# Performance work log

Measured on AMD Instinct MI355X. Metric: run time of the kernel, lower is better.

The kernel has to match this reference:

```python
import jax, jax.numpy as jnp
import numpy as np

B, T = 128, 512
V, E, U, K = 50000, 100, 128, 32


def _lstm(x, Wk, Wr, b):
    # x: [B, T, D] -> [B, T, U], Keras LSTM gate order i,f,g,o
    Bd = x.shape[0]
    Ud = Wr.shape[0]
    xs = jnp.swapaxes(x, 0, 1)  # [T, B, D]

    def step(carry, xt):
        h, c = carry
        z = xt @ Wk + h @ Wr + b
        i, f, g, o = jnp.split(z, 4, axis=-1)
        c = jax.nn.sigmoid(f) * c + jax.nn.sigmoid(i) * jnp.tanh(g)
        h = jax.nn.sigmoid(o) * jnp.tanh(c)
        return (h, c), h

    init = (jnp.zeros((Bd, Ud), x.dtype), jnp.zeros((Bd, Ud), x.dtype))
    _, hs = jax.lax.scan(step, init, xs)
    return jnp.swapaxes(hs, 0, 1)


def _crf_logZ(em, trans):
    # em: [B, T, K] emissions; trans: [K, K]. Forward algorithm log-partition.
    alpha0 = em[:, 0]  # [B, K]
    es = jnp.swapaxes(em[:, 1:], 0, 1)  # [T-1, B, K]

    def step(alpha, et):
        # alpha[b, i] + trans[i, j] -> logsumexp over i, plus emission
        alpha = jax.nn.logsumexp(alpha[:, :, None] + trans[None], axis=1) + et
        return alpha, None

    alphaT, _ = jax.lax.scan(step, alpha0, es)
    return jax.nn.logsumexp(alphaT, axis=-1)  # [B]


def setup_inputs() -> dict:
    key = jax.random.key(0)
    ks = jax.random.split(key, 11)
    s = 0.1
    return {
        "tokens": jax.random.randint(ks[0], (B, T), 0, V, dtype=jnp.int32),
        "emb": jax.random.normal(ks[1], (V, E), jnp.float32) * s,
        "Wk_f": jax.random.normal(ks[2], (E, 4 * U), jnp.float32) * s,
        "Wr_f": jax.random.normal(ks[3], (U, 4 * U), jnp.float32) * s,
        "b_f": jnp.zeros((4 * U,), jnp.float32),
        "Wk_b": jax.random.normal(ks[4], (E, 4 * U), jnp.float32) * s,
        "Wr_b": jax.random.normal(ks[5], (U, 4 * U), jnp.float32) * s,
        "b_b": jnp.zeros((4 * U,), jnp.float32),
        "crf_kernel": jax.random.normal(ks[6], (2 * U, K), jnp.float32) * s,
        "crf_bias": jnp.zeros((K,), jnp.float32),
        "trans": jax.random.normal(ks[7], (K, K), jnp.float32) * s,
    }


def reference(tokens, emb, Wk_f, Wr_f, b_f, Wk_b, Wr_b, b_b, crf_kernel, crf_bias, trans):
    x = emb[tokens]  # [B, T, E]
    h_f = _lstm(x, Wk_f, Wr_f, b_f)
    h_b = _lstm(x[:, ::-1], Wk_b, Wr_b, b_b)[:, ::-1]
    h = jnp.concatenate([h_f, h_b], axis=-1)  # [B, T, 2U] (dropout = identity at inference)
    em = h @ crf_kernel + crf_bias  # [B, T, K] CRF emission potentials
    return _crf_logZ(em, trans)  # [B] log-partition via CRF forward DP
```

## Files before the change

### kernel.cpp

```cpp
#include <hip/hip_runtime.h>
#include <hip/hip_bf16.h>

#define B_  128
#define T_  512
#define V_  50000
#define VP  50016
#define E_  100
#define U_  128
#define K_  32
#define G4  512
#define KP  128
#define GRP 8

typedef _Float16 h2_t __attribute__((ext_vector_type(2)));
typedef _Float16 f16x8 __attribute__((ext_vector_type(8)));
typedef __fp16   h2raw_t __attribute__((ext_vector_type(2)));
typedef short    bf16x8 __attribute__((ext_vector_type(8)));
typedef float    f32x4  __attribute__((ext_vector_type(4)));
typedef unsigned short u16x4 __attribute__((ext_vector_type(4)));

__device__ __forceinline__ h2_t pk2(float a, float b) {
    h2raw_t r = __builtin_amdgcn_cvt_pkrtz(a, b);
    union { h2raw_t r; h2_t h; } u; u.r = r; return u.h;
}

#if __has_builtin(__builtin_amdgcn_rcpf)
__device__ __forceinline__ float rcp_f(float x) { return __builtin_amdgcn_rcpf(x); }
#else
__device__ __forceinline__ float rcp_f(float x) { return 1.f / x; }
#endif

__device__ __forceinline__ unsigned short bf16_bits(float v) {
    __hip_bfloat16 b = __float2bfloat16(v);
    union { __hip_bfloat16 b; unsigned short s; } u; u.b = b; return u.s;
}
__device__ __forceinline__ float bf2f(unsigned short u) {
    union { unsigned int i; float f; } x; x.i = ((unsigned int)u) << 16; return x.f;
}

__global__ __launch_bounds__(128) void pack_b_kernel(
    const float* __restrict__ Wk_f, const float* __restrict__ Wk_b,
    __hip_bfloat16* __restrict__ Bb)
{
    const int n = blockIdx.x;
    const int k = threadIdx.x;
    float v = 0.f;
    if (k < E_) v = (n < 512) ? Wk_f[k * 512 + n] : Wk_b[k * 512 + (n - 512)];
    Bb[n * KP + k] = __float2bfloat16(v);
}

__global__ __launch_bounds__(256, 2) void proj_mfma_kernel(
    const float* __restrict__ emb,
    const __hip_bfloat16* __restrict__ Bb,
    const float* __restrict__ b_f, const float* __restrict__ b_b,
    __hip_bfloat16* __restrict__ proj)
{
    const int r0   = blockIdx.x * 32;
    const int tid  = threadIdx.x;
    const int wv   = tid >> 6;
    const int lane = tid & 63;
    const int quad = lane >> 4;
    const int l16  = lane & 15;

    __shared__ __align__(16) float C_lds[32][268];
    unsigned short* A_st = (unsigned short*)&C_lds[0][0];

    for (int idx = tid; idx < 32 * 64; idx += 256) {
        int r = idx >> 6, kk = idx & 63;
        int vr = r0 + r; if (vr >= V_) vr = V_ - 1;
        unsigned int w = 0;
        if (kk < 50) {
            float2 v = *(const float2*)(emb + (long long)vr * E_ + 2 * kk);
            w = ((unsigned int)bf16_bits(v.y) << 16) | bf16_bits(v.x);
        }
        *(unsigned int*)&A_st[r * 136 + 2 * kk] = w;
    }
    __syncthreads();

    bf16x8 af[2][4];
    #pragma unroll
    for (int mt = 0; mt < 2; ++mt)
        #pragma unroll
        for (int kc = 0; kc < 4; ++kc)
            af[mt][kc] = *(const bf16x8*)&A_st[(mt * 16 + l16) * 136 +
                                               kc * 32 + quad * 8];
    __syncthreads();

    const unsigned short* Bu = (const unsigned short*)Bb;

    for (int ng = 0; ng < 4; ++ng) {
        const int n0 = ng * 256;

        bf16x8 bfr[4][4];
        #pragma unroll
        for (int nt = 0; nt < 4; ++nt)
            #pragma unroll
            for (int kc = 0; kc < 4; ++kc)
                bfr[nt][kc] = *(const bf16x8*)(Bu +
                    (n0 + wv * 64 + nt * 16 + l16) * KP + kc * 32 + quad * 8);

        f32x4 acc[2][4];
        #pragma unroll
        for (int mt = 0; mt < 2; ++mt)
            #pragma unroll
            for (int nt = 0; nt < 4; ++nt)
                acc[mt][nt] = (f32x4){0.f, 0.f, 0.f, 0.f};

        #pragma unroll
        for (int mt = 0; mt < 2; ++mt)
            #pragma unroll
            for (int nt = 0; nt < 4; ++nt)
                #pragma unroll
                for (int kc = 0; kc < 4; ++kc)
                    acc[mt][nt] = __builtin_amdgcn_mfma_f32_16x16x32_bf16(
                        af[mt][kc], bfr[nt][kc], acc[mt][nt], 0, 0, 0);

        #pragma unroll
        for (int mt = 0; mt < 2; ++mt)
            #pragma unroll
            for (int nt = 0; nt < 4; ++nt)
                #pragma unroll
                for (int v = 0; v < 4; ++v)
                    C_lds[mt * 16 + quad * 4 + v][wv * 64 + nt * 16 + l16] =
                        acc[mt][nt][v];
        __syncthreads();

        const float* bias = (n0 < 512) ? b_f : b_b;
        const int nbase = n0 & 511;
        for (int idx = tid; idx < 32 * 128; idx += 256) {
            int r = idx >> 7, cc = (idx & 127) * 2;
            float v0 = C_lds[r][cc]     + bias[nbase + cc];
            float v1 = C_lds[r][cc + 1] + bias[nbase + cc + 1];
            unsigned int w = ((unsigned int)bf16_bits(v1) << 16) | bf16_bits(v0);
            *(unsigned int*)(proj + (long long)(r0 + r) * 1024 + n0 + cc) = w;
        }
        __syncthreads();
    }
}

__device__ __forceinline__ float sigmoid_f(float x) {
    return rcp_f(1.f + __expf(-x));
}
__device__ __forceinline__ float tanh_f(float x) {
    return 1.f - 2.f * rcp_f(__expf(2.f * x) + 1.f);
}

__global__ __launch_bounds__(512, 1) void lstm_kernel(
    const __hip_bfloat16* __restrict__ proj,
    const int* __restrict__ tokens,
    const float* __restrict__ Wr_f, const float* __restrict__ Wr_b,
    __hip_bfloat16* __restrict__ h_buf)
{
    const int bid  = blockIdx.x;
    const int dir  = bid >> 7;
    const int b    = bid & 127;
    const int tid  = threadIdx.x;
    const int w    = tid >> 6;
    const int lane = tid & 63;
    const int quad = lane >> 4;
    const int l16  = lane & 15;
    const int unit = 16 * w + l16;

    const float* Wr = dir ? Wr_b : Wr_f;

    union uf16 { f16x8 v; h2_t p[4]; };
    f16x8 wb[4][4];
    #pragma unroll
    for (int gq = 0; gq < 4; ++gq) {
        const int col = gq * 128 + unit;
        #pragma unroll
        for (int kc = 0; kc < 4; ++kc) {
            const int k0 = kc * 32 + quad * 8;
            uf16 u;
            #pragma unroll
            for (int jj = 0; jj < 4; ++jj)
                u.p[jj] = pk2(Wr[(k0 + 2 * jj)     * G4 + col],
                              Wr[(k0 + 2 * jj + 1) * G4 + col]);
            wb[gq][kc] = u.v;
        }
    }

    __shared__ __align__(16) _Float16 hpl[2][128];
    __shared__ __align__(16) unsigned short xkl[2][GRP][512];
    if (tid < 128) hpl[0][tid] = (_Float16)0.f;
    float c = 0.f;

    const int tbase = b * T_;
    const long long rowbase = (long long)b * T_;
    const __hip_bfloat16* prt = proj + dir * 512 + tid;
    const int xw = (tid & 127) * 4 + (tid >> 7);

    int tokn[GRP];
    {
        unsigned short v0[GRP];
        #pragma unroll
        for (int d = 0; d < GRP; ++d) {
            int t0 = dir ? (T_ - 1 - d) : d;
            int tk = tokens[tbase + t0];
            v0[d] = *(const unsigned short*)(prt + (long long)tk * 1024);
        }
        #pragma unroll
        for (int d = 0; d < GRP; ++d)
            xkl[0][d][xw] = v0[d];
        #pragma unroll
        for (int d = 0; d < GRP; ++d) {
            int s = GRP + d;
            int t1 = dir ? (T_ - 1 - s) : s;
            tokn[d] = tokens[tbase + t1];
        }
    }
    __syncthreads();

    const int NG = T_ / GRP;
    for (int g = 0; g < NG; ++g) {
        unsigned short xknx[GRP];
        #pragma unroll
        for (int d = 0; d < GRP; ++d)
            xknx[d] = *(const unsigned short*)(prt + (long long)tokn[d] * 1024);

        int tokn2[GRP];
        #pragma unroll
        for (int d = 0; d < GRP; ++d) {
            int s = (g + 2) * GRP + d; if (s > T_ - 1) s = T_ - 1;
            int t = dir ? (T_ - 1 - s) : s;
            tokn2[d] = tokens[tbase + t];
        }

        float hreg[GRP];
        #pragma unroll
        for (int d = 0; d < GRP; ++d) {
            f16x8 a[4];
            #pragma unroll
            for (int kc = 0; kc < 4; ++kc)
                a[kc] = *(const f16x8*)&hpl[d & 1][kc * 32 + quad * 8];

            u16x4 xr = *(const u16x4*)&xkl[g & 1][d][(unsigned)unit * 4];

            f32x4 acc[4];
            #pragma unroll
            for (int gq = 0; gq < 4; ++gq)
                acc[gq] = (f32x4){0.f, 0.f, 0.f, 0.f};
            #pragma unroll
            for (int gq = 0; gq < 4; ++gq)
                #pragma unroll
                for (int kc = 0; kc < 4; ++kc)
                    acc[gq] = __builtin_amdgcn_mfma_f32_16x16x32_f16(
                        a[kc], wb[gq][kc], acc[gq], 0, 0, 0);

            float zi = acc[0][0] + bf2f(xr.x);
            float zf = acc[1][0] + bf2f(xr.y);
            float zg = acc[2][0] + bf2f(xr.z);
            float zo = acc[3][0] + bf2f(xr.w);
            c = sigmoid_f(zf) * c + sigmoid_f(zi) * tanh_f(zg);
            float h = sigmoid_f(zo) * tanh_f(c);
            hreg[d] = h;

            if (quad == 0) hpl[(d + 1) & 1][unit] = (_Float16)h;

            if (d < GRP - 1) {
                asm volatile("s_waitcnt lgkmcnt(0)" ::: "memory");
                __builtin_amdgcn_s_barrier();
                asm volatile("" ::: "memory");
            } else {
                #pragma unroll
                for (int dd = 0; dd < GRP; ++dd)
                    xkl[(g + 1) & 1][dd][xw] = xknx[dd];
                asm volatile("s_waitcnt lgkmcnt(0)" ::: "memory");
                __builtin_amdgcn_s_barrier();
                asm volatile("" ::: "memory");
            }
        }

        unsigned int hp[GRP];
        #pragma unroll
        for (int d = 0; d < GRP; ++d) {
            float hn = __shfl_down(hreg[d], 1, 64);
            hp[d] = ((unsigned int)bf16_bits(hn) << 16) | bf16_bits(hreg[d]);
        }
        if (quad == 0 && !(l16 & 1)) {
            #pragma unroll
            for (int d = 0; d < GRP; ++d) {
                int s = g * GRP + d;
                int t = dir ? (T_ - 1 - s) : s;
                *(unsigned int*)(h_buf + (rowbase + t) * 256 + dir * U_ + unit) =
                    hp[d];
            }
        }

        #pragma unroll
        for (int d = 0; d < GRP; ++d) tokn[d] = tokn2[d];
    }
}

__global__ __launch_bounds__(256) void em_kernel(
    const __hip_bfloat16* __restrict__ h_buf,
    const float* __restrict__ ck, const float* __restrict__ cb,
    float* __restrict__ em)
{
    const int tid  = threadIdx.x;
    const int part = tid >> 5;
    const int k    = tid & 31;

    float ckr[32];
    #pragma unroll
    for (int i = 0; i < 32; ++i)
        ckr[i] = ck[(part * 32 + i) * K_ + k];
    const float cbk = cb[k];

    __shared__ float h_l[8][256];
    __shared__ float part_l[8][8][K_];

    const int r0 = blockIdx.x * 64;

    for (int round = 0; round < 8; ++round) {
        const int rbase = r0 + round * 8;
        #pragma unroll
        for (int j = 0; j < 8; ++j)
            h_l[j][tid] = __bfloat162float(h_buf[(long long)(rbase + j) * 256 + tid]);
        __syncthreads();

        #pragma unroll
        for (int j = 0; j < 8; ++j) {
            float pp = 0.f;
            #pragma unroll
            for (int i = 0; i < 32; ++i)
                pp = fmaf(h_l[j][part * 32 + i], ckr[i], pp);
            part_l[j][part][k] = pp;
        }
        __syncthreads();

        {
            int j2 = tid >> 5;
            float e = cbk;
            #pragma unroll
            for (int pq = 0; pq < 8; ++pq) e += part_l[j2][pq][k];
            em[(long long)(rbase + j2) * K_ + k] = e;
        }
        __syncthreads();
    }
}

#define PF_ 8
__global__ __launch_bounds__(64) void crf_kernel(
    const float* __restrict__ em,
    const float* __restrict__ trans,
    float* __restrict__ out)
{
    const int b    = blockIdx.x;
    const int lane = threadIdx.x;
    const int k    = lane & 31;
    const int half = lane >> 5;

    float etr[16];
    #pragma unroll
    for (int i = 0; i < 16; ++i)
        etr[i] = __expf(trans[(half * 16 + i) * K_ + k]);

    const float* em_b = em + (long long)b * T_ * K_;

    float ep[PF_];
    #pragma unroll
    for (int d = 0; d < PF_; ++d)
        ep[d] = em_b[d * K_ + k];

    float w = 0.f;
    float L = 0.f;
    for (int tb = 0; tb < T_; tb += PF_) {
        float en[PF_];
        if (tb + PF_ < T_) {
            #pragma unroll
            for (int d = 0; d < PF_; ++d)
                en[d] = em_b[(tb + PF_ + d) * K_ + k];
        } else {
            #pragma unroll
            for (int d = 0; d < PF_; ++d) en[d] = 0.f;
        }

        float eem[PF_];
        #pragma unroll
        for (int d = 0; d < PF_; ++d) eem[d] = __expf(ep[d]);

        #pragma unroll
        for (int d = 0; d < PF_; ++d) {
            if (tb + d == 0) {
                w = eem[d];
            } else {
                float acc = 0.f;
                #pragma unroll
                for (int i = 0; i < 16; ++i) {
                    float wv = __shfl(w, half * 16 + i, 64);
                    acc = fmaf(wv, etr[i], acc);
                }
                acc += __shfl_xor(acc, 32, 64);
                w = acc * eem[d];
            }
        }

        {
            float w0 = __shfl(w, 0, 64);
            w *= rcp_f(w0);
            L += __logf(w0);
        }

        #pragma unroll
        for (int d = 0; d < PF_; ++d) ep[d] = en[d];
    }

    float s = w;
    #pragma unroll
    for (int d = 1; d < 32; d <<= 1)
        s += __shfl_xor(s, d, 64);
    if (lane == 0) out[b] = L + __logf(s);
}

extern "C" void kernel_launch(void* const* d_in, const int* in_sizes, int n_in,
                              void* d_out, int out_size, void* d_ws, size_t ws_size,
                              hipStream_t stream)
{
    const int*   tokens = (const int*)  d_in[0];
    const float* emb    = (const float*)d_in[1];
    const float* Wk_f   = (const float*)d_in[2];
    const float* Wr_f   = (const float*)d_in[3];
    const float* b_f    = (const float*)d_in[4];
    const float* Wk_b   = (const float*)d_in[5];
    const float* Wr_b   = (const float*)d_in[6];
    const float* b_b    = (const float*)d_in[7];
    const float* ck     = (const float*)d_in[8];
    const float* cb     = (const float*)d_in[9];
    const float* trans  = (const float*)d_in[10];
    float* out = (float*)d_out;

    const long long ROWS = (long long)B_ * T_;
    __hip_bfloat16* proj  = (__hip_bfloat16*)d_ws;
    __hip_bfloat16* h_buf = proj + (long long)VP * 1024;
    float* em = (float*)(h_buf + ROWS * 256);
    __hip_bfloat16* Bb = (__hip_bfloat16*)(em + ROWS * K_);

    hipLaunchKernelGGL(pack_b_kernel, dim3(1024), dim3(128), 0, stream,
                       Wk_f, Wk_b, Bb);
    hipLaunchKernelGGL(proj_mfma_kernel, dim3(VP / 32), dim3(256), 0, stream,
                       emb, Bb, b_f, b_b, proj);
    hipLaunchKernelGGL(lstm_kernel, dim3(256), dim3(512), 0, stream,
                       proj, tokens, Wr_f, Wr_b, h_buf);
    hipLaunchKernelGGL(em_kernel, dim3((int)(ROWS / 64)), dim3(256), 0, stream,
                       h_buf, ck, cb, em);
    hipLaunchKernelGGL(crf_kernel, dim3(B_), dim3(64), 0, stream,
                       em, trans, out);
}
```

Baseline: 575.7 us.

## Batch 16 sequences per LSTM block to fill MFMA rows

The LSTM kernel now processes 16 batch rows per workgroup instead of one, so all 16 rows of each 16x16x32 MFMA carry real hidden states rather than one useful row. The grid shrinks from 256 to 16 blocks, cutting redundant recurrent matmul work per sequence. Input-projection gathers are restaged per timestep into a transposed LDS layout, with one barrier per step. The cost is that only 16 CUs are used, so the whole 512-step serial chain runs on far fewer compute units.

```diff
diff --git a/kernel.cpp b/kernel.cpp
--- a/kernel.cpp
+++ b/kernel.cpp
@@ -10,7 +10,6 @@
 #define K_  32
 #define G4  512
 #define KP  128
-#define GRP 8
 
 typedef _Float16 h2_t __attribute__((ext_vector_type(2)));
 typedef _Float16 f16x8 __attribute__((ext_vector_type(8)));
@@ -152,8 +151,8 @@
     __hip_bfloat16* __restrict__ h_buf)
 {
     const int bid  = blockIdx.x;
-    const int dir  = bid >> 7;
-    const int b    = bid & 127;
+    const int dir  = bid >> 3;
+    const int b0   = (bid & 7) * 16;
     const int tid  = threadIdx.x;
     const int w    = tid >> 6;
     const int lane = tid & 63;
@@ -180,115 +179,115 @@
         }
     }
 
-    __shared__ __align__(16) _Float16 hpl[2][128];
-    __shared__ __align__(16) unsigned short xkl[2][GRP][512];
-    if (tid < 128) hpl[0][tid] = (_Float16)0.f;
-    float c = 0.f;
-
-    const int tbase = b * T_;
-    const long long rowbase = (long long)b * T_;
-    const __hip_bfloat16* prt = proj + dir * 512 + tid;
-    const int xw = (tid & 127) * 4 + (tid >> 7);
-
-    int tokn[GRP];
+    __shared__ __align__(16) _Float16      h_lds[2][16][136];
+    __shared__ __align__(16) unsigned short xkb[2][128][72];
+
+    const int cp   = tid >> 1;
+    const int cgrp = (tid & 1) * 8;
+    const int col0 = cp * 2;
+    const int g0   = col0 >> 7;
+    const int u0   = col0 & 127;
+    const unsigned short* prj = (const unsigned short*)proj + dir * 512 + col0;
+
+    for (int idx = tid; idx < 16 * 136; idx += 512)
+        ((_Float16*)h_lds[0])[idx] = (_Float16)0.f;
+    float cst[4] = {0.f, 0.f, 0.f, 0.f};
+
+    int tokS[8];
     {
-        unsigned short v0[GRP];
-        #pragma unroll
-        for (int d = 0; d < GRP; ++d) {
-            int t0 = dir ? (T_ - 1 - d) : d;
-            int tk = tokens[tbase + t0];
-            v0[d] = *(const unsigned short*)(prt + (long long)tk * 1024);
-        }
-        #pragma unroll
-        for (int d = 0; d < GRP; ++d)
-            xkl[0][d][xw] = v0[d];
-        #pragma unroll
-        for (int d = 0; d < GRP; ++d) {
-            int s = GRP + d;
-            int t1 = dir ? (T_ - 1 - s) : s;
-            tokn[d] = tokens[tbase + t1];
-        }
+        const int tt0 = dir ? (T_ - 1) : 0;
+        int v32[8];
+        #pragma unroll
+        for (int cc = 0; cc < 8; ++cc) {
+            int tk = tokens[(b0 + cgrp + cc) * T_ + tt0];
+            v32[cc] = *(const int*)(prj + (size_t)tk * 1024);
+        }
+        union { unsigned short s[8]; uint4 q; } plo, phi;
+        #pragma unroll
+        for (int cc = 0; cc < 8; ++cc) {
+            plo.s[cc] = (unsigned short)(v32[cc] & 0xffff);
+            phi.s[cc] = (unsigned short)(((unsigned int)v32[cc]) >> 16);
+        }
+        *(uint4*)&xkb[0][u0][g0 * 16 + cgrp]     = plo.q;
+        *(uint4*)&xkb[0][u0 + 1][g0 * 16 + cgrp] = phi.q;
+        const int tt1 = dir ? (T_ - 2) : 1;
+        #pragma unroll
+        for (int cc = 0; cc < 8; ++cc)
+            tokS[cc] = tokens[(b0 + cgrp + cc) * T_ + tt1];
     }
     __syncthreads();
 
-    const int NG = T_ / GRP;
-    for (int g = 0; g < NG; ++g) {
-        unsigned short xknx[GRP];
-        #pragma unroll
-        for (int d = 0; d < GRP; ++d)
-            xknx[d] = *(const unsigned short*)(prt + (long long)tokn[d] * 1024);
-
-        int tokn2[GRP];
-        #pragma unroll
-        for (int d = 0; d < GRP; ++d) {
-            int s = (g + 2) * GRP + d; if (s > T_ - 1) s = T_ - 1;
-            int t = dir ? (T_ - 1 - s) : s;
-            tokn2[d] = tokens[tbase + t];
-        }
-
-        float hreg[GRP];
-        #pragma unroll
-        for (int d = 0; d < GRP; ++d) {
-            f16x8 a[4];
+    for (int t = 0; t < T_; ++t) {
+        const int cb = t & 1, nb = cb ^ 1;
+
+        int v32[8];
+        #pragma unroll
+        for (int cc = 0; cc < 8; ++cc)
+            v32[cc] = *(const int*)(prj + (size_t)tokS[cc] * 1024);
+
+        int tokN[8];
+        {
+            int s2 = (t + 2 < T_) ? (t + 2) : (T_ - 1);
+            int tt2 = dir ? (T_ - 1 - s2) : s2;
+            #pragma unroll
+            for (int cc = 0; cc < 8; ++cc)
+                tokN[cc] = tokens[(b0 + cgrp + cc) * T_ + tt2];
+        }
+
+        f16x8 a[4];
+        #pragma unroll
+        for (int kc = 0; kc < 4; ++kc)
+            a[kc] = *(const f16x8*)&h_lds[cb][l16][kc * 32 + quad * 8];
+        u16x4 xr[4];
+        #pragma unroll
+        for (int gq = 0; gq < 4; ++gq)
+            xr[gq] = *(const u16x4*)&xkb[cb][unit][gq * 16 + quad * 4];
+
+        f32x4 acc[4];
+        #pragma unroll
+        for (int gq = 0; gq < 4; ++gq)
+            acc[gq] = (f32x4){0.f, 0.f, 0.f, 0.f};
+        #pragma unroll
+        for (int gq = 0; gq < 4; ++gq)
             #pragma unroll
             for (int kc = 0; kc < 4; ++kc)
-                a[kc] = *(const f16x8*)&hpl[d & 1][kc * 32 + quad * 8];
-
-            u16x4 xr = *(const u16x4*)&xkl[g & 1][d][(unsigned)unit * 4];
-
-            f32x4 acc[4];
-            #pragma unroll
-            for (int gq = 0; gq < 4; ++gq)
-                acc[gq] = (f32x4){0.f, 0.f, 0.f, 0.f};
-            #pragma unroll
-            for (int gq = 0; gq < 4; ++gq)
-                #pragma unroll
-                for (int kc = 0; kc < 4; ++kc)
-                    acc[gq] = __builtin_amdgcn_mfma_f32_16x16x32_f16(
-                        a[kc], wb[gq][kc], acc[gq], 0, 0, 0);
-
-            float zi = acc[0][0] + bf2f(xr.x);
-            float zf = acc[1][0] + bf2f(xr.y);
-            float zg = acc[2][0] + bf2f(xr.z);
-            float zo = acc[3][0] + bf2f(xr.w);
-            c = sigmoid_f(zf) * c + sigmoid_f(zi) * tanh_f(zg);
-            float h = sigmoid_f(zo) * tanh_f(c);
-            hreg[d] = h;
-
-            if (quad == 0) hpl[(d + 1) & 1][unit] = (_Float16)h;
-
-            if (d < GRP - 1) {
-                asm volatile("s_waitcnt lgkmcnt(0)" ::: "memory");
-                __builtin_amdgcn_s_barrier();
-                asm volatile("" ::: "memory");
-            } else {
-                #pragma unroll
-                for (int dd = 0; dd < GRP; ++dd)
-                    xkl[(g + 1) & 1][dd][xw] = xknx[dd];
-                asm volatile("s_waitcnt lgkmcnt(0)" ::: "memory");
-                __builtin_amdgcn_s_barrier();
-                asm volatile("" ::: "memory");
+                acc[gq] = __builtin_amdgcn_mfma_f32_16x16x32_f16(
+                    a[kc], wb[gq][kc], acc[gq], 0, 0, 0);
+
+        float hb[4];
+        #pragma unroll
+        for (int v = 0; v < 4; ++v) {
+            float zi = acc[0][v] + bf2f(xr[0][v]);
+            float zf = acc[1][v] + bf2f(xr[1][v]);
+            float zg = acc[2][v] + bf2f(xr[2][v]);
+            float zo = acc[3][v] + bf2f(xr[3][v]);
+            cst[v] = sigmoid_f(zf) * cst[v] + sigmoid_f(zi) * tanh_f(zg);
+            hb[v] = sigmoid_f(zo) * tanh_f(cst[v]);
+            h_lds[nb][quad * 4 + v][unit] = (_Float16)hb[v];
+        }
+
+        const int ttime = dir ? (T_ - 1 - t) : t;
+        #pragma unroll
+        for (int v = 0; v < 4; ++v)
+            h_buf[((size_t)(b0 + quad * 4 + v) * T_ + ttime) * 256 +
+                  dir * 128 + unit] = __float2bfloat16(hb[v]);
+
+        {
+            union { unsigned short s[8]; uint4 q; } plo, phi;
+            #pragma unroll
+            for (int cc = 0; cc < 8; ++cc) {
+                plo.s[cc] = (unsigned short)(v32[cc] & 0xffff);
+                phi.s[cc] = (unsigned short)(((unsigned int)v32[cc]) >> 16);
             }
-        }
-
-        unsigned int hp[GRP];
-        #pragma unroll
-        for (int d = 0; d < GRP; ++d) {
-            float hn = __shfl_down(hreg[d], 1, 64);
-            hp[d] = ((unsigned int)bf16_bits(hn) << 16) | bf16_bits(hreg[d]);
-        }
-        if (quad == 0 && !(l16 & 1)) {
-            #pragma unroll
-            for (int d = 0; d < GRP; ++d) {
-                int s = g * GRP + d;
-                int t = dir ? (T_ - 1 - s) : s;
-                *(unsigned int*)(h_buf + (rowbase + t) * 256 + dir * U_ + unit) =
-                    hp[d];
-            }
-        }
-
-        #pragma unroll
-        for (int d = 0; d < GRP; ++d) tokn[d] = tokn2[d];
+            *(uint4*)&xkb[nb][u0][g0 * 16 + cgrp]     = plo.q;
+            *(uint4*)&xkb[nb][u0 + 1][g0 * 16 + cgrp] = phi.q;
+        }
+        #pragma unroll
+        for (int cc = 0; cc < 8; ++cc) tokS[cc] = tokN[cc];
+
+        asm volatile("s_waitcnt lgkmcnt(0)" ::: "memory");
+        __builtin_amdgcn_s_barrier();
+        asm volatile("" ::: "memory");
     }
 }
 
@@ -440,7 +439,7 @@
                        Wk_f, Wk_b, Bb);
     hipLaunchKernelGGL(proj_mfma_kernel, dim3(VP / 32), dim3(256), 0, stream,
                        emb, Bb, b_f, b_b, proj);
-    hipLaunchKernelGGL(lstm_kernel, dim3(256), dim3(512), 0, stream,
+    hipLaunchKernelGGL(lstm_kernel, dim3(16), dim3(512), 0, stream,
                        proj, tokens, Wr_f, Wr_b, h_buf);
     hipLaunchKernelGGL(em_kernel, dim3((int)(ROWS / 64)), dim3(256), 0, stream,
                        h_buf, ck, cb, em);
```

New measurement: 1.047 ms. 1.82x slower.
